# Optimization experiments

Measured on AMD Instinct MI355X. Metric: run time of the kernel, lower is better.

Reference implementation:

```python
import jax, jax.numpy as jnp
import numpy as np

# dims matching init_kwargs
L = 2          # lstm_depth
H = 512        # lstm_size
E = 512        # text_embedding_size
V = 32000      # vocab_size
FH = 512       # feature_embedding_hidden_size
FEAT = 2048    # feature_size
START_IDX = 3.0  # start_of_seq_token_idx (used as a fill value, per original code)


def _lstm_cell(x, h, c, Wih, Whh, b):
    # PyTorch gate order: i, f, g, o. Wih:[in,4H], Whh:[H,4H], b:[4H]
    gates = x @ Wih + h @ Whh + b  # [B,4H]
    i, f, g, o = jnp.split(gates, 4, axis=-1)
    c_new = jax.nn.sigmoid(f) * c + jax.nn.sigmoid(i) * jnp.tanh(g)
    h_new = jax.nn.sigmoid(o) * jnp.tanh(c_new)
    return h_new, c_new


def setup_inputs() -> dict:
    key = jax.random.key(0)
    ks = jax.random.split(key, 12)
    B, N, T = 64, 49, 40
    s = 0.02
    img_data = jax.random.normal(ks[0], (B, N, FEAT), jnp.float32)
    W_fh = jax.random.normal(ks[1], (FEAT, FH), jnp.float32) * s
    b_fh = jnp.zeros((FH,), jnp.float32)
    Wc = jax.random.normal(ks[2], (L, FH, H), jnp.float32) * s
    bc = jnp.zeros((L, H), jnp.float32)
    Wh = jax.random.normal(ks[3], (L, FH, H), jnp.float32) * s
    bh = jnp.zeros((L, H), jnp.float32)
    W_ih = jax.random.normal(ks[4], (L, E, 4 * H), jnp.float32) * 0.04
    W_hh = jax.random.normal(ks[5], (L, H, 4 * H), jnp.float32) * 0.04
    b_lstm = jnp.zeros((L, 4 * H), jnp.float32)
    emb = jax.random.normal(ks[6], (V, E), jnp.float32) * s
    u = jax.random.uniform(ks[7], (T, B, V), jnp.float32, minval=1e-6, maxval=1.0 - 1e-6)
    gumbel = -jnp.log(-jnp.log(u))  # Gumbel(0,1) noise: Gumbel-max == Categorical.sample
    return {
        "img_data": img_data, "W_fh": W_fh, "b_fh": b_fh,
        "Wc": Wc, "bc": bc, "Wh": Wh, "bh": bh,
        "W_ih": W_ih, "W_hh": W_hh, "b_lstm": b_lstm,
        "emb": emb, "gumbel": gumbel, "max_seq_len": 40,
    }


def reference(img_data, W_fh, b_fh, Wc, bc, Wh, bh, W_ih, W_hh, b_lstm, emb, gumbel, max_seq_len):
    B = img_data.shape[0]
    # f_embedding = tanh(Linear(img_data)) : [B,N,FH]
    f_emb = jnp.tanh(img_data @ W_fh + b_fh)
    # mean over regions commutes with the per-layer Linear: mean(f @ W + b) = mean(f) @ W + b
    f_mean = jnp.mean(f_emb, axis=1)  # [B,FH]
    c0 = jnp.einsum('bf,lfh->lbh', f_mean, Wc) + bc[:, None, :]  # [L,B,H]
    h0 = jnp.einsum('bf,lfh->lbh', f_mean, Wh) + bh[:, None, :]
    # initial "embedding" is zeros + start_of_seq_token_idx (a constant fill, per original)
    x0 = jnp.full((B, E), START_IDX, dtype=img_data.dtype)
    emb_T = emb.T  # [E,V]

    def step(carry, g_t):
        h, c, x = carry  # h,c:[L,B,H], x:[B,E]; g_t:[B,V]
        inp = x
        hs, cs = [], []
        for l in range(L):  # small static depth
            hn, cn = _lstm_cell(inp, h[l], c[l], W_ih[l], W_hh[l], b_lstm[l])
            hs.append(hn); cs.append(cn)
            inp = hn
        logits = inp @ emb_T                      # [B,V]
        logp = jax.nn.log_softmax(logits, axis=-1)
        tok = jnp.argmax(logp + g_t, axis=-1)     # Gumbel-max categorical sample
        lp = jnp.take_along_axis(logp, tok[:, None], axis=1)[:, 0]  # [B]
        x_next = emb[tok]                         # next-step embedding lookup
        return (jnp.stack(hs, 0), jnp.stack(cs, 0), x_next), (tok, lp)

    _, (tokens, log_probs) = jax.lax.scan(step, (h0, c0, x0), gumbel)
    return tokens.T, log_probs.T  # [B,T], [B,T]
```

## Files before the change

### kernel.cpp

```cpp
#include <hip/hip_runtime.h>
#include <cmath>

namespace {

constexpr int BATCH = 64;
constexpr int NREG  = 49;
constexpr int FEATN = 2048;
constexpr int FHN   = 512;
constexpr int HID   = 512;
constexpr int EMBN  = 512;
constexpr int VOC   = 32000;
constexpr int TSTEPS= 40;
constexpr int G4    = 2048;
constexpr int NVT   = VOC / 128;

typedef short bf16x8 __attribute__((ext_vector_type(8)));
typedef float f32x4  __attribute__((ext_vector_type(4)));

__device__ __forceinline__ float sigm(float x) { return 1.0f / (1.0f + expf(-x)); }

__device__ __forceinline__ unsigned short f2bf(float f) {
  unsigned u = __float_as_uint(f);
  unsigned r = (u + 0x7fffu + ((u >> 16) & 1u)) >> 16;
  return (unsigned short)r;
}

__device__ __forceinline__ bool better(float a, int ia, float b, int ib) {
  return a > b || (a == b && ia < ib);
}
__device__ __forceinline__ void top2_merge(float& v1, int& i1, float& v2, int& i2,
                                           float u1, int j1, float u2, int j2) {
  if (better(u1, j1, v1, i1)) {
    float t = v1; int ti = i1;
    v1 = u1; i1 = j1;
    if (better(u2, j2, t, ti)) { v2 = u2; i2 = j2; } else { v2 = t; i2 = ti; }
  } else {
    if (better(u1, j1, v2, i2)) { v2 = u1; i2 = j1; }
  }
}
__device__ __forceinline__ void lse_merge(float& m, float& s, float om, float os) {
  float nm = fmaxf(m, om);
  float ns = 0.f;
  if (m  > -INFINITY) ns += s  * expf(m  - nm);
  if (om > -INFINITY) ns += os * expf(om - nm);
  m = nm; s = ns;
}

__global__ __launch_bounds__(256) void k_feat(const float* __restrict__ img, const float* __restrict__ W,
                                              const float* __restrict__ bias, float* __restrict__ femb) {
  const int m0 = blockIdx.x * 64, n0 = blockIdx.y * 64;
  __shared__ float As[16][68];
  __shared__ float Bs[16][68];
  const int tid = threadIdx.x, tx = tid & 15, ty = tid >> 4;
  float acc[4][4] = {};
  for (int k0 = 0; k0 < FEATN; k0 += 16) {
#pragma unroll
    for (int e = 0; e < 4; ++e) {
      int idx = tid + e * 256, m = idx >> 4, k = idx & 15;
      As[k][m] = img[(size_t)(m0 + m) * FEATN + k0 + k];
    }
#pragma unroll
    for (int e = 0; e < 4; ++e) {
      int idx = tid + e * 256, k = idx >> 6, n = idx & 63;
      Bs[k][n] = W[(size_t)(k0 + k) * FHN + n0 + n];
    }
    __syncthreads();
#pragma unroll
    for (int k = 0; k < 16; ++k) {
      float4 av = *(const float4*)&As[k][ty * 4];
      float4 bv = *(const float4*)&Bs[k][tx * 4];
      float a[4] = {av.x, av.y, av.z, av.w}, b[4] = {bv.x, bv.y, bv.z, bv.w};
#pragma unroll
      for (int i = 0; i < 4; ++i)
#pragma unroll
        for (int j = 0; j < 4; ++j) acc[i][j] = fmaf(a[i], b[j], acc[i][j]);
    }
    __syncthreads();
  }
#pragma unroll
  for (int i = 0; i < 4; ++i) {
    int m = m0 + ty * 4 + i, n = n0 + tx * 4;
    float4 o;
    o.x = tanhf(acc[i][0] + bias[n + 0]);
    o.y = tanhf(acc[i][1] + bias[n + 1]);
    o.z = tanhf(acc[i][2] + bias[n + 2]);
    o.w = tanhf(acc[i][3] + bias[n + 3]);
    *(float4*)&femb[(size_t)m * FHN + n] = o;
  }
}

__global__ void k_mean(const float* __restrict__ femb, float* __restrict__ fmean) {
  const int gid = blockIdx.x * 256 + threadIdx.x;
  const int b = gid >> 9, f = gid & 511;
  float s = 0.f;
  for (int n = 0; n < NREG; ++n) s += femb[(size_t)(b * NREG + n) * FHN + f];
  fmean[gid] = s * (1.0f / NREG);
}

__global__ __launch_bounds__(256) void k_h0c0(const float* __restrict__ fmean,
    const float* __restrict__ Wc, const float* __restrict__ bc,
    const float* __restrict__ Wh, const float* __restrict__ bh,
    float* __restrict__ hbuf, float* __restrict__ cbuf) {
  const int n0 = blockIdx.x * 64, l = blockIdx.y, isH = blockIdx.z;
  const float* W   = (isH ? Wh : Wc) + (size_t)l * FHN * HID;
  const float* bias= (isH ? bh : bc) + l * HID;
  float* outp      = (isH ? hbuf : cbuf) + (size_t)l * BATCH * HID;
  __shared__ float As[16][68], Bs[16][68];
  const int tid = threadIdx.x, tx = tid & 15, ty = tid >> 4;
  float acc[4][4] = {};
  for (int k0 = 0; k0 < FHN; k0 += 16) {
#pragma unroll
    for (int e = 0; e < 4; ++e) { int idx = tid + e * 256, m = idx >> 4, k = idx & 15; As[k][m] = fmean[m * FHN + k0 + k]; }
#pragma unroll
    for (int e = 0; e < 4; ++e) { int idx = tid + e * 256, k = idx >> 6, n = idx & 63; Bs[k][n] = W[(size_t)(k0 + k) * HID + n0 + n]; }
    __syncthreads();
#pragma unroll
    for (int k = 0; k < 16; ++k) {
      float4 av = *(const float4*)&As[k][ty * 4];
      float4 bv = *(const float4*)&Bs[k][tx * 4];
      float a[4] = {av.x, av.y, av.z, av.w}, b[4] = {bv.x, bv.y, bv.z, bv.w};
#pragma unroll
      for (int i = 0; i < 4; ++i)
#pragma unroll
        for (int j = 0; j < 4; ++j) acc[i][j] = fmaf(a[i], b[j], acc[i][j]);
    }
    __syncthreads();
  }
#pragma unroll
  for (int i = 0; i < 4; ++i) {
    int m = ty * 4 + i, n = n0 + tx * 4;
    float4 o = make_float4(acc[i][0] + bias[n], acc[i][1] + bias[n + 1],
                           acc[i][2] + bias[n + 2], acc[i][3] + bias[n + 3]);
    *(float4*)&outp[(size_t)m * HID + n] = o;
  }
}

__global__ void k_init(float* __restrict__ xbuf) {
  xbuf[blockIdx.x * 256 + threadIdx.x] = 3.0f;
}

__global__ void k_emb2bf(const float* __restrict__ emb, unsigned short* __restrict__ ebf) {
  const int i = blockIdx.x * 256 + threadIdx.x;
  const float4* p = reinterpret_cast<const float4*>(emb) + (size_t)i * 2;
  float4 a = p[0], b = p[1];
  uint4 o;
  o.x = (unsigned)f2bf(a.x) | ((unsigned)f2bf(a.y) << 16);
  o.y = (unsigned)f2bf(a.z) | ((unsigned)f2bf(a.w) << 16);
  o.z = (unsigned)f2bf(b.x) | ((unsigned)f2bf(b.y) << 16);
  o.w = (unsigned)f2bf(b.z) | ((unsigned)f2bf(b.w) << 16);
  reinterpret_cast<uint4*>(ebf)[i] = o;
}

__global__ __launch_bounds__(256) void k_gates(const float* __restrict__ X, const float* __restrict__ Hs,
    const float* __restrict__ Wih, const float* __restrict__ Whh, float* __restrict__ part) {
  const int n0 = blockIdx.x * 64;
  const int ks = blockIdx.y;
  const float* A; const float* Wm; int kbase;
  if (ks < 4) { A = X;  Wm = Wih; kbase = ks * 128; }
  else        { A = Hs; Wm = Whh; kbase = (ks - 4) * 128; }
  __shared__ float As[16][68], Bs[16][68];
  const int tid = threadIdx.x, tx = tid & 15, ty = tid >> 4;
  float acc[4][4] = {};
  for (int kk = 0; kk < 128; kk += 16) {
    const int k0 = kbase + kk;
#pragma unroll
    for (int e = 0; e < 4; ++e) { int idx = tid + e * 256, m = idx >> 4, k = idx & 15; As[k][m] = A[m * EMBN + k0 + k]; }
#pragma unroll
    for (int e = 0; e < 4; ++e) { int idx = tid + e * 256, k = idx >> 6, n = idx & 63; Bs[k][n] = Wm[(size_t)(k0 + k) * G4 + n0 + n]; }
    __syncthreads();
#pragma unroll
    for (int k = 0; k < 16; ++k) {
      float4 av = *(const float4*)&As[k][ty * 4];
      float4 bvv = *(const float4*)&Bs[k][tx * 4];
      float a[4] = {av.x, av.y, av.z, av.w}, b[4] = {bvv.x, bvv.y, bvv.z, bvv.w};
#pragma unroll
      for (int i = 0; i < 4; ++i)
#pragma unroll
        for (int j = 0; j < 4; ++j) acc[i][j] = fmaf(a[i], b[j], acc[i][j]);
    }
    __syncthreads();
  }
  float* pp = part + (size_t)ks * BATCH * G4;
#pragma unroll
  for (int i = 0; i < 4; ++i) {
    int m = ty * 4 + i, n = n0 + tx * 4;
    *(float4*)&pp[(size_t)m * G4 + n] = make_float4(acc[i][0], acc[i][1], acc[i][2], acc[i][3]);
  }
}

__global__ void k_cell(const float* __restrict__ part, const float* __restrict__ bias,
                       float* __restrict__ h, float* __restrict__ c,
                       unsigned short* __restrict__ hbf) {
  const int gid = blockIdx.x * 256 + threadIdx.x;
  const int b = gid >> 9, j = gid & 511;
  float gi = bias[j], gf = bias[j + 512], gg = bias[j + 1024], go = bias[j + 1536];
#pragma unroll
  for (int ks = 0; ks < 8; ++ks) {
    const float* p = part + (size_t)ks * BATCH * G4 + (size_t)b * G4;
    gi += p[j]; gf += p[j + 512]; gg += p[j + 1024]; go += p[j + 1536];
  }
  float cn = sigm(gf) * c[gid] + sigm(gi) * tanhf(gg);
  float hn = sigm(go) * tanhf(cn);
  c[gid] = cn; h[gid] = hn;
  if (hbf) hbf[gid] = f2bf(hn);
}

__global__ __launch_bounds__(256) void k_logits_mfma(
    const unsigned short* __restrict__ embbf,
    const unsigned short* __restrict__ h1bf,
    const float* __restrict__ gum,
    float* __restrict__ red) {
  const int v0 = blockIdx.x * 128;
  const int tid = threadIdx.x;
  const int lane = tid & 63, w = tid >> 6;
  const int l15 = lane & 15, l4 = lane >> 4;

  __shared__ unsigned short hl[32768];
  __shared__ float rm_[256], rs_[256], rv1_[256], rv2_[256];
  __shared__ int   ri1_[256], ri2_[256];

#pragma unroll
  for (int i = 0; i < 16; ++i) {
    int c = tid + i * 256;
    int row = c >> 6;
    int inb = (c & 63) << 4;
    uint4 v = *reinterpret_cast<const uint4*>(h1bf + ((size_t)c << 3));
    int sw = inb ^ ((row & 7) << 4);
    *reinterpret_cast<uint4*>(reinterpret_cast<char*>(hl) + row * 1024 + sw) = v;
  }
  __syncthreads();

  f32x4 acc[2][4];
#pragma unroll
  for (int m = 0; m < 2; ++m)
#pragma unroll
    for (int n = 0; n < 4; ++n) acc[m][n] = (f32x4){0.f, 0.f, 0.f, 0.f};

  const unsigned short* aptr = embbf + (size_t)(v0 + w * 32 + l15) * 512 + l4 * 8;
#pragma unroll
  for (int ks = 0; ks < 16; ++ks) {
    bf16x8 a0 = *reinterpret_cast<const bf16x8*>(aptr + ks * 32);
    bf16x8 a1 = *reinterpret_cast<const bf16x8*>(aptr + 16 * 512 + ks * 32);
    bf16x8 bb[4];
#pragma unroll
    for (int n = 0; n < 4; ++n) {
      int row = n * 16 + l15;
      int inb = ks * 64 + l4 * 16;
      int sw = inb ^ ((row & 7) << 4);
      bb[n] = *reinterpret_cast<const bf16x8*>(reinterpret_cast<const char*>(hl) + row * 1024 + sw);
    }
#pragma unroll
    for (int n = 0; n < 4; ++n) {
      acc[0][n] = __builtin_amdgcn_mfma_f32_16x16x32_bf16(a0, bb[n], acc[0][n], 0, 0, 0);
      acc[1][n] = __builtin_amdgcn_mfma_f32_16x16x32_bf16(a1, bb[n], acc[1][n], 0, 0, 0);
    }
  }

  const int vb = v0 + w * 32 + l4 * 4;
#pragma unroll
  for (int n = 0; n < 4; ++n) {
    const int b = n * 16 + l15;
    const float* gb = gum + (size_t)b * VOC + vb;
    float4 g0 = *reinterpret_cast<const float4*>(gb);
    float4 g1 = *reinterpret_cast<const float4*>(gb + 16);
    float lg[8] = {acc[0][n][0], acc[0][n][1], acc[0][n][2], acc[0][n][3],
                   acc[1][n][0], acc[1][n][1], acc[1][n][2], acc[1][n][3]};
    float gv[8] = {g0.x, g0.y, g0.z, g0.w, g1.x, g1.y, g1.z, g1.w};
    float mx = lg[0];
#pragma unroll
    for (int i = 1; i < 8; ++i) mx = fmaxf(mx, lg[i]);
    float ss = 0.f;
    float v1 = -INFINITY, v2 = -INFINITY; int i1 = 0x7fffffff, i2 = 0x7fffffff;
#pragma unroll
    for (int i = 0; i < 8; ++i) {
      ss += expf(lg[i] - mx);
      float val = lg[i] + gv[i];
      int idx = vb + (i & 3) + ((i >> 2) << 4);
      if (better(val, idx, v1, i1)) { v2 = v1; i2 = i1; v1 = val; i1 = idx; }
      else if (better(val, idx, v2, i2)) { v2 = val; i2 = idx; }
    }
#pragma unroll
    for (int mask = 16; mask <= 32; mask <<= 1) {
      float om = __shfl_xor(mx, mask);
      float os = __shfl_xor(ss, mask);
      float u1 = __shfl_xor(v1, mask); int j1 = __shfl_xor(i1, mask);
      float u2 = __shfl_xor(v2, mask); int j2 = __shfl_xor(i2, mask);
      lse_merge(mx, ss, om, os);
      top2_merge(v1, i1, v2, i2, u1, j1, u2, j2);
    }
    if (lane < 16) {
      int slot = (w * 4 + n) * 16 + l15;
      rm_[slot] = mx; rs_[slot] = ss;
      rv1_[slot] = v1; ri1_[slot] = i1; rv2_[slot] = v2; ri2_[slot] = i2;
    }
  }
  __syncthreads();
  if (tid < 64) {
    const int n = tid >> 4, c = tid & 15;
    int s0 = n * 16 + c;
    float M = rm_[s0], S = rs_[s0], V1 = rv1_[s0], V2 = rv2_[s0];
    int I1 = ri1_[s0], I2 = ri2_[s0];
#pragma unroll
    for (int ww = 1; ww < 4; ++ww) {
      int sl = (ww * 4 + n) * 16 + c;
      lse_merge(M, S, rm_[sl], rs_[sl]);
      top2_merge(V1, I1, V2, I2, rv1_[sl], ri1_[sl], rv2_[sl], ri2_[sl]);
    }
    float* rp = red + ((size_t)blockIdx.x * 64 + tid) * 8;
    rp[0] = M; rp[1] = S;
    rp[2] = V1; rp[3] = __int_as_float(I1);
    rp[4] = V2; rp[5] = __int_as_float(I2);
  }
}

__global__ __launch_bounds__(256) void k_sample(const float* __restrict__ red,
    const float* __restrict__ emb, const float* __restrict__ h1f, const float* __restrict__ gum,
    float* __restrict__ xnext, float* __restrict__ out, int t) {
  const int b = blockIdx.x, tid = threadIdx.x;
  __shared__ float rm[256], rs[256], rv1[256], rv2[256];
  __shared__ int   ri1[256], ri2[256];
  float m = -INFINITY, s = 0.f, v1 = -INFINITY, v2 = -INFINITY;
  int i1 = 0x7fffffff, i2 = 0x7fffffff;
  if (tid < NVT) {
    const float* rp = red + ((size_t)tid * 64 + b) * 8;
    m = rp[0]; s = rp[1];
    v1 = rp[2]; i1 = __float_as_int(rp[3]);
    v2 = rp[4]; i2 = __float_as_int(rp[5]);
  }
  rm[tid] = m; rs[tid] = s; rv1[tid] = v1; ri1[tid] = i1; rv2[tid] = v2; ri2[tid] = i2;
  __syncthreads();
  for (int off = 128; off > 0; off >>= 1) {
    if (tid < off) {
      float M = rm[tid], S = rs[tid];
      lse_merge(M, S, rm[tid + off], rs[tid + off]);
      rm[tid] = M; rs[tid] = S;
      float a1 = rv1[tid], a2 = rv2[tid]; int c1 = ri1[tid], c2 = ri2[tid];
      top2_merge(a1, c1, a2, c2, rv1[tid + off], ri1[tid + off], rv2[tid + off], ri2[tid + off]);
      rv1[tid] = a1; ri1[tid] = c1; rv2[tid] = a2; ri2[tid] = c2;
    }
    __syncthreads();
  }
  const int I1 = ri1[0], I2 = ri2[0];
  const float lse = rm[0] + logf(rs[0]);
  __shared__ float s1[256], s2[256];
  const float* e1 = emb + (size_t)I1 * EMBN;
  const float* e2 = emb + (size_t)I2 * EMBN;
  const float* hb = h1f + b * EMBN;
  float d1 = 0.f, d2 = 0.f;
  for (int k = tid; k < EMBN; k += 256) {
    float hv = hb[k];
    d1 = fmaf(e1[k], hv, d1);
    d2 = fmaf(e2[k], hv, d2);
  }
  s1[tid] = d1; s2[tid] = d2;
  __syncthreads();
  for (int off = 128; off > 0; off >>= 1) {
    if (tid < off) { s1[tid] += s1[tid + off]; s2[tid] += s2[tid + off]; }
    __syncthreads();
  }
  const float x1 = s1[0] + gum[(size_t)b * VOC + I1];
  const float x2 = s2[0] + gum[(size_t)b * VOC + I2];
  int tok; float dsel;
  if (x2 > x1 || (x2 == x1 && I2 < I1)) { tok = I2; dsel = s2[0]; }
  else                                  { tok = I1; dsel = s1[0]; }
  const float* et = emb + (size_t)tok * EMBN;
  for (int k = tid; k < EMBN; k += 256) xnext[b * EMBN + k] = et[k];
  if (tid == 0) {
    out[b * TSTEPS + t] = (float)tok;
    out[BATCH * TSTEPS + b * TSTEPS + t] = dsel - lse;
  }
}

}

extern "C" void kernel_launch(void* const* d_in, const int* in_sizes, int n_in,
                              void* d_out, int out_size, void* d_ws, size_t ws_size,
                              hipStream_t stream) {
  const float* img  = (const float*)d_in[0];
  const float* W_fh = (const float*)d_in[1];
  const float* b_fh = (const float*)d_in[2];
  const float* Wc   = (const float*)d_in[3];
  const float* bc   = (const float*)d_in[4];
  const float* Wh   = (const float*)d_in[5];
  const float* bh   = (const float*)d_in[6];
  const float* W_ih = (const float*)d_in[7];
  const float* W_hh = (const float*)d_in[8];
  const float* b_l  = (const float*)d_in[9];
  const float* emb  = (const float*)d_in[10];
  const float* gum  = (const float*)d_in[11];
  float* out = (float*)d_out;

  float* w     = (float*)d_ws;
  float* femb  = w;
  float* fmean = femb + (size_t)3136 * 512;
  float* hbuf  = fmean + 64 * 512;
  float* cbuf  = hbuf + 2 * 64 * 512;
  float* xbuf  = cbuf + 2 * 64 * 512;
  float* part  = xbuf + 64 * 512;
  float* red   = part + (size_t)8 * 64 * 2048;
  unsigned short* embbf = (unsigned short*)(red + 250 * 64 * 8);
  unsigned short* h1bf  = embbf + (size_t)VOC * EMBN;

  k_feat<<<dim3(49, 8), 256, 0, stream>>>(img, W_fh, b_fh, femb);
  k_mean<<<128, 256, 0, stream>>>(femb, fmean);
  k_h0c0<<<dim3(8, 2, 2), 256, 0, stream>>>(fmean, Wc, bc, Wh, bh, hbuf, cbuf);
  k_init<<<128, 256, 0, stream>>>(xbuf);
  k_emb2bf<<<8000, 256, 0, stream>>>(emb, embbf);

  for (int t = 0; t < TSTEPS; ++t) {
    const float* gum_t = gum + (size_t)t * BATCH * VOC;
    k_gates<<<dim3(32, 8), 256, 0, stream>>>(xbuf, hbuf, W_ih, W_hh, part);
    k_cell<<<128, 256, 0, stream>>>(part, b_l, hbuf, cbuf, (unsigned short*)nullptr);
    k_gates<<<dim3(32, 8), 256, 0, stream>>>(hbuf, hbuf + 64 * 512,
                                             W_ih + (size_t)512 * 2048, W_hh + (size_t)512 * 2048, part);
    k_cell<<<128, 256, 0, stream>>>(part, b_l + 2048, hbuf + 64 * 512, cbuf + 64 * 512, h1bf);
    k_logits_mfma<<<NVT, 256, 0, stream>>>(embbf, h1bf, gum_t, red);
    k_sample<<<64, 256, 0, stream>>>(red, emb, hbuf + 64 * 512, gum_t, xbuf, out, t);
  }
}
```

Measured before the change: 2.216 ms.

## Use split-bf16 MFMA for feature and LSTM gate GEMMs

Replaces the fp32 FMA tiled GEMMs for the image-feature projection and the per-step LSTM gate matmuls with bf16 MFMA kernels. Precision is kept by splitting each operand into hi+lo bf16 parts and summing three products. Weights are pre-transposed and split once per call, and activations (x, h) are written as hi/lo bf16 by the producing kernels. This adds preprocessing passes over the image tensor and weights, plus extra workspace and memory traffic, in exchange for matrix-core throughput.

```diff
diff --git a/kernel.cpp b/kernel.cpp
--- a/kernel.cpp
+++ b/kernel.cpp
@@ -24,6 +24,9 @@
   unsigned r = (u + 0x7fffu + ((u >> 16) & 1u)) >> 16;
   return (unsigned short)r;
 }
+__device__ __forceinline__ float bf2f(unsigned short h) {
+  return __uint_as_float(((unsigned)h) << 16);
+}
 
 __device__ __forceinline__ bool better(float a, int ia, float b, int ib) {
   return a > b || (a == b && ia < ib);
@@ -46,47 +49,89 @@
   m = nm; s = ns;
 }
 
-__global__ __launch_bounds__(256) void k_feat(const float* __restrict__ img, const float* __restrict__ W,
-                                              const float* __restrict__ bias, float* __restrict__ femb) {
+__global__ __launch_bounds__(256) void k_trans(const float* __restrict__ src,
+    unsigned short* __restrict__ dhi, unsigned short* __restrict__ dlo, int K, int N) {
+  __shared__ float tile[32][33];
+  const int k0 = blockIdx.x * 32, n0 = blockIdx.y * 32;
+  const int tx = threadIdx.x & 31, ty = threadIdx.x >> 5;
+#pragma unroll
+  for (int r = ty; r < 32; r += 8) tile[r][tx] = src[(size_t)(k0 + r) * N + n0 + tx];
+  __syncthreads();
+#pragma unroll
+  for (int r = ty; r < 32; r += 8) {
+    float v = tile[tx][r];
+    unsigned short hv = f2bf(v);
+    size_t o = (size_t)(n0 + r) * K + k0 + tx;
+    dhi[o] = hv;
+    dlo[o] = f2bf(v - bf2f(hv));
+  }
+}
+
+__global__ void k_split(const float* __restrict__ src, unsigned short* __restrict__ dhi,
+                        unsigned short* __restrict__ dlo) {
+  const size_t i = (size_t)blockIdx.x * 256 + threadIdx.x;
+  const float4* p = reinterpret_cast<const float4*>(src) + i * 2;
+  float4 a = p[0], b = p[1];
+  float v[8] = {a.x, a.y, a.z, a.w, b.x, b.y, b.z, b.w};
+  unsigned short hi[8], lo[8];
+#pragma unroll
+  for (int j = 0; j < 8; ++j) {
+    hi[j] = f2bf(v[j]);
+    lo[j] = f2bf(v[j] - bf2f(hi[j]));
+  }
+  uint4 oh, ol;
+  oh.x = hi[0] | (hi[1] << 16); oh.y = hi[2] | (hi[3] << 16);
+  oh.z = hi[4] | (hi[5] << 16); oh.w = hi[6] | (hi[7] << 16);
+  ol.x = lo[0] | (lo[1] << 16); ol.y = lo[2] | (lo[3] << 16);
+  ol.z = lo[4] | (lo[5] << 16); ol.w = lo[6] | (lo[7] << 16);
+  reinterpret_cast<uint4*>(dhi)[i] = oh;
+  reinterpret_cast<uint4*>(dlo)[i] = ol;
+}
+
+__global__ void k_emb2bf(const float* __restrict__ emb, unsigned short* __restrict__ ebf) {
+  const size_t i = (size_t)blockIdx.x * 256 + threadIdx.x;
+  const float4* p = reinterpret_cast<const float4*>(emb) + i * 2;
+  float4 a = p[0], b = p[1];
+  uint4 o;
+  o.x = (unsigned)f2bf(a.x) | ((unsigned)f2bf(a.y) << 16);
+  o.y = (unsigned)f2bf(a.z) | ((unsigned)f2bf(a.w) << 16);
+  o.z = (unsigned)f2bf(b.x) | ((unsigned)f2bf(b.y) << 16);
+  o.w = (unsigned)f2bf(b.z) | ((unsigned)f2bf(b.w) << 16);
+  reinterpret_cast<uint4*>(ebf)[i] = o;
+}
+
+__global__ __launch_bounds__(256) void k_feat_mfma(
+    const unsigned short* __restrict__ Ahi, const unsigned short* __restrict__ Alo,
+    const unsigned short* __restrict__ Bhi, const unsigned short* __restrict__ Blo,
+    const float* __restrict__ bias, float* __restrict__ femb) {
   const int m0 = blockIdx.x * 64, n0 = blockIdx.y * 64;
-  __shared__ float As[16][68];
-  __shared__ float Bs[16][68];
-  const int tid = threadIdx.x, tx = tid & 15, ty = tid >> 4;
-  float acc[4][4] = {};
-  for (int k0 = 0; k0 < FEATN; k0 += 16) {
-#pragma unroll
-    for (int e = 0; e < 4; ++e) {
-      int idx = tid + e * 256, m = idx >> 4, k = idx & 15;
-      As[k][m] = img[(size_t)(m0 + m) * FEATN + k0 + k];
-    }
-#pragma unroll
-    for (int e = 0; e < 4; ++e) {
-      int idx = tid + e * 256, k = idx >> 6, n = idx & 63;
-      Bs[k][n] = W[(size_t)(k0 + k) * FHN + n0 + n];
-    }
-    __syncthreads();
-#pragma unroll
-    for (int k = 0; k < 16; ++k) {
-      float4 av = *(const float4*)&As[k][ty * 4];
-      float4 bv = *(const float4*)&Bs[k][tx * 4];
-      float a[4] = {av.x, av.y, av.z, av.w}, b[4] = {bv.x, bv.y, bv.z, bv.w};
-#pragma unroll
-      for (int i = 0; i < 4; ++i)
-#pragma unroll
-        for (int j = 0; j < 4; ++j) acc[i][j] = fmaf(a[i], b[j], acc[i][j]);
-    }
-    __syncthreads();
-  }
-#pragma unroll
-  for (int i = 0; i < 4; ++i) {
-    int m = m0 + ty * 4 + i, n = n0 + tx * 4;
-    float4 o;
-    o.x = tanhf(acc[i][0] + bias[n + 0]);
-    o.y = tanhf(acc[i][1] + bias[n + 1]);
-    o.z = tanhf(acc[i][2] + bias[n + 2]);
-    o.w = tanhf(acc[i][3] + bias[n + 3]);
-    *(float4*)&femb[(size_t)m * FHN + n] = o;
-  }
+  const int tid = threadIdx.x, lane = tid & 63, w = tid >> 6;
+  const int l15 = lane & 15, l4 = lane >> 4;
+  f32x4 acc[4];
+#pragma unroll
+  for (int nt = 0; nt < 4; ++nt) acc[nt] = (f32x4){0.f, 0.f, 0.f, 0.f};
+  const size_t arow = (size_t)(m0 + w * 16 + l15) * FEATN;
+  for (int kk = 0; kk < FEATN / 32; ++kk) {
+    const int k = kk * 32 + l4 * 8;
+    bf16x8 a1 = *reinterpret_cast<const bf16x8*>(Ahi + arow + k);
+    bf16x8 a2 = *reinterpret_cast<const bf16x8*>(Alo + arow + k);
+#pragma unroll
+    for (int nt = 0; nt < 4; ++nt) {
+      const size_t brow = (size_t)(n0 + nt * 16 + l15) * FEATN + k;
+      bf16x8 b1 = *reinterpret_cast<const bf16x8*>(Bhi + brow);
+      bf16x8 b2 = *reinterpret_cast<const bf16x8*>(Blo + brow);
+      acc[nt] = __builtin_amdgcn_mfma_f32_16x16x32_bf16(a1, b1, acc[nt], 0, 0, 0);
+      acc[nt] = __builtin_amdgcn_mfma_f32_16x16x32_bf16(a1, b2, acc[nt], 0, 0, 0);
+      acc[nt] = __builtin_amdgcn_mfma_f32_16x16x32_bf16(a2, b1, acc[nt], 0, 0, 0);
+    }
+  }
+#pragma unroll
+  for (int nt = 0; nt < 4; ++nt)
+#pragma unroll
+    for (int i = 0; i < 4; ++i) {
+      int m = m0 + w * 16 + l4 * 4 + i, n = n0 + nt * 16 + l15;
+      femb[(size_t)m * FHN + n] = tanhf(acc[nt][i] + bias[n]);
+    }
 }
 
 __global__ void k_mean(const float* __restrict__ femb, float* __restrict__ fmean) {
@@ -100,7 +145,8 @@
 __global__ __launch_bounds__(256) void k_h0c0(const float* __restrict__ fmean,
     const float* __restrict__ Wc, const float* __restrict__ bc,
     const float* __restrict__ Wh, const float* __restrict__ bh,
-    float* __restrict__ hbuf, float* __restrict__ cbuf) {
+    float* __restrict__ hbuf, float* __restrict__ cbuf,
+    unsigned short* __restrict__ hshi, unsigned short* __restrict__ hslo) {
   const int n0 = blockIdx.x * 64, l = blockIdx.y, isH = blockIdx.z;
   const float* W   = (isH ? Wh : Wc) + (size_t)l * FHN * HID;
   const float* bias= (isH ? bh : bc) + l * HID;
@@ -129,68 +175,73 @@
 #pragma unroll
   for (int i = 0; i < 4; ++i) {
     int m = ty * 4 + i, n = n0 + tx * 4;
-    float4 o = make_float4(acc[i][0] + bias[n], acc[i][1] + bias[n + 1],
-                           acc[i][2] + bias[n + 2], acc[i][3] + bias[n + 3]);
-    *(float4*)&outp[(size_t)m * HID + n] = o;
-  }
-}
-
-__global__ void k_init(float* __restrict__ xbuf) {
-  xbuf[blockIdx.x * 256 + threadIdx.x] = 3.0f;
-}
-
-__global__ void k_emb2bf(const float* __restrict__ emb, unsigned short* __restrict__ ebf) {
+    float vals[4];
+#pragma unroll
+    for (int j = 0; j < 4; ++j) vals[j] = acc[i][j] + bias[n + j];
+    *(float4*)&outp[(size_t)m * HID + n] = make_float4(vals[0], vals[1], vals[2], vals[3]);
+    if (isH) {
+#pragma unroll
+      for (int j = 0; j < 4; ++j) {
+        unsigned short hv = f2bf(vals[j]);
+        size_t o = (size_t)l * BATCH * HID + (size_t)m * HID + n + j;
+        hshi[o] = hv;
+        hslo[o] = f2bf(vals[j] - bf2f(hv));
+      }
+    }
+  }
+}
+
+__global__ void k_initx(unsigned short* __restrict__ xhi, unsigned short* __restrict__ xlo) {
   const int i = blockIdx.x * 256 + threadIdx.x;
-  const float4* p = reinterpret_cast<const float4*>(emb) + (size_t)i * 2;
-  float4 a = p[0], b = p[1];
-  uint4 o;
-  o.x = (unsigned)f2bf(a.x) | ((unsigned)f2bf(a.y) << 16);
-  o.y = (unsigned)f2bf(a.z) | ((unsigned)f2bf(a.w) << 16);
-  o.z = (unsigned)f2bf(b.x) | ((unsigned)f2bf(b.y) << 16);
-  o.w = (unsigned)f2bf(b.z) | ((unsigned)f2bf(b.w) << 16);
-  reinterpret_cast<uint4*>(ebf)[i] = o;
-}
-
-__global__ __launch_bounds__(256) void k_gates(const float* __restrict__ X, const float* __restrict__ Hs,
-    const float* __restrict__ Wih, const float* __restrict__ Whh, float* __restrict__ part) {
+  xhi[i] = 0x4040; xlo[i] = 0;
+}
+
+__global__ __launch_bounds__(256) void k_gates_mfma(
+    const unsigned short* __restrict__ xhi, const unsigned short* __restrict__ xlo,
+    const unsigned short* __restrict__ hhi, const unsigned short* __restrict__ hlo,
+    const unsigned short* __restrict__ wih_hi, const unsigned short* __restrict__ wih_lo,
+    const unsigned short* __restrict__ whh_hi, const unsigned short* __restrict__ whh_lo,
+    float* __restrict__ part) {
   const int n0 = blockIdx.x * 64;
   const int ks = blockIdx.y;
-  const float* A; const float* Wm; int kbase;
-  if (ks < 4) { A = X;  Wm = Wih; kbase = ks * 128; }
-  else        { A = Hs; Wm = Whh; kbase = (ks - 4) * 128; }
-  __shared__ float As[16][68], Bs[16][68];
-  const int tid = threadIdx.x, tx = tid & 15, ty = tid >> 4;
-  float acc[4][4] = {};
-  for (int kk = 0; kk < 128; kk += 16) {
-    const int k0 = kbase + kk;
-#pragma unroll
-    for (int e = 0; e < 4; ++e) { int idx = tid + e * 256, m = idx >> 4, k = idx & 15; As[k][m] = A[m * EMBN + k0 + k]; }
-#pragma unroll
-    for (int e = 0; e < 4; ++e) { int idx = tid + e * 256, k = idx >> 6, n = idx & 63; Bs[k][n] = Wm[(size_t)(k0 + k) * G4 + n0 + n]; }
-    __syncthreads();
-#pragma unroll
-    for (int k = 0; k < 16; ++k) {
-      float4 av = *(const float4*)&As[k][ty * 4];
-      float4 bvv = *(const float4*)&Bs[k][tx * 4];
-      float a[4] = {av.x, av.y, av.z, av.w}, b[4] = {bvv.x, bvv.y, bvv.z, bvv.w};
-#pragma unroll
-      for (int i = 0; i < 4; ++i)
-#pragma unroll
-        for (int j = 0; j < 4; ++j) acc[i][j] = fmaf(a[i], b[j], acc[i][j]);
-    }
-    __syncthreads();
+  const unsigned short *Ah, *Al, *Wh_, *Wl;
+  int kbase;
+  if (ks < 4) { Ah = xhi; Al = xlo; Wh_ = wih_hi; Wl = wih_lo; kbase = ks * 128; }
+  else        { Ah = hhi; Al = hlo; Wh_ = whh_hi; Wl = whh_lo; kbase = (ks - 4) * 128; }
+  const int tid = threadIdx.x, lane = tid & 63, w = tid >> 6;
+  const int l15 = lane & 15, l4 = lane >> 4;
+  f32x4 acc[4];
+#pragma unroll
+  for (int nt = 0; nt < 4; ++nt) acc[nt] = (f32x4){0.f, 0.f, 0.f, 0.f};
+  const size_t arow = (size_t)(w * 16 + l15) * EMBN;
+#pragma unroll
+  for (int kk = 0; kk < 4; ++kk) {
+    const int k = kbase + kk * 32 + l4 * 8;
+    bf16x8 a1 = *reinterpret_cast<const bf16x8*>(Ah + arow + k);
+    bf16x8 a2 = *reinterpret_cast<const bf16x8*>(Al + arow + k);
+#pragma unroll
+    for (int nt = 0; nt < 4; ++nt) {
+      const size_t brow = (size_t)(n0 + nt * 16 + l15) * EMBN + k;
+      bf16x8 b1 = *reinterpret_cast<const bf16x8*>(Wh_ + brow);
+      bf16x8 b2 = *reinterpret_cast<const bf16x8*>(Wl + brow);
+      acc[nt] = __builtin_amdgcn_mfma_f32_16x16x32_bf16(a1, b1, acc[nt], 0, 0, 0);
+      acc[nt] = __builtin_amdgcn_mfma_f32_16x16x32_bf16(a1, b2, acc[nt], 0, 0, 0);
+      acc[nt] = __builtin_amdgcn_mfma_f32_16x16x32_bf16(a2, b1, acc[nt], 0, 0, 0);
+    }
   }
   float* pp = part + (size_t)ks * BATCH * G4;
 #pragma unroll
-  for (int i = 0; i < 4; ++i) {
-    int m = ty * 4 + i, n = n0 + tx * 4;
-    *(float4*)&pp[(size_t)m * G4 + n] = make_float4(acc[i][0], acc[i][1], acc[i][2], acc[i][3]);
-  }
+  for (int nt = 0; nt < 4; ++nt)
+#pragma unroll
+    for (int i = 0; i < 4; ++i) {
+      int b = w * 16 + l4 * 4 + i, n = n0 + nt * 16 + l15;
+      pp[(size_t)b * G4 + n] = acc[nt][i];
+    }
 }
 
 __global__ void k_cell(const float* __restrict__ part, const float* __restrict__ bias,
                        float* __restrict__ h, float* __restrict__ c,
-                       unsigned short* __restrict__ hbf) {
+                       unsigned short* __restrict__ hhi, unsigned short* __restrict__ hlo) {
   const int gid = blockIdx.x * 256 + threadIdx.x;
   const int b = gid >> 9, j = gid & 511;
   float gi = bias[j], gf = bias[j + 512], gg = bias[j + 1024], go = bias[j + 1536];
@@ -202,7 +253,9 @@
   float cn = sigm(gf) * c[gid] + sigm(gi) * tanhf(gg);
   float hn = sigm(go) * tanhf(cn);
   c[gid] = cn; h[gid] = hn;
-  if (hbf) hbf[gid] = f2bf(hn);
+  unsigned short hv = f2bf(hn);
+  hhi[gid] = hv;
+  hlo[gid] = f2bf(hn - bf2f(hv));
 }
 
 __global__ __launch_bounds__(256) void k_logits_mfma(
@@ -315,7 +368,8 @@
 
 __global__ __launch_bounds__(256) void k_sample(const float* __restrict__ red,
     const float* __restrict__ emb, const float* __restrict__ h1f, const float* __restrict__ gum,
-    float* __restrict__ xnext, float* __restrict__ out, int t) {
+    unsigned short* __restrict__ xhi, unsigned short* __restrict__ xlo,
+    float* __restrict__ out, int t) {
   const int b = blockIdx.x, tid = threadIdx.x;
   __shared__ float rm[256], rs[256], rv1[256], rv2[256];
   __shared__ int   ri1[256], ri2[256];
@@ -364,7 +418,12 @@
   if (x2 > x1 || (x2 == x1 && I2 < I1)) { tok = I2; dsel = s2[0]; }
   else                                  { tok = I1; dsel = s1[0]; }
   const float* et = emb + (size_t)tok * EMBN;
-  for (int k = tid; k < EMBN; k += 256) xnext[b * EMBN + k] = et[k];
+  for (int k = tid; k < EMBN; k += 256) {
+    float ev = et[k];
+    unsigned short hv = f2bf(ev);
+    xhi[b * EMBN + k] = hv;
+    xlo[b * EMBN + k] = f2bf(ev - bf2f(hv));
+  }
   if (tid == 0) {
     out[b * TSTEPS + t] = (float)tok;
     out[BATCH * TSTEPS + b * TSTEPS + t] = dsel - lse;
@@ -395,26 +454,48 @@
   float* fmean = femb + (size_t)3136 * 512;
   float* hbuf  = fmean + 64 * 512;
   float* cbuf  = hbuf + 2 * 64 * 512;
-  float* xbuf  = cbuf + 2 * 64 * 512;
-  float* part  = xbuf + 64 * 512;
+  float* part  = cbuf + 2 * 64 * 512;
   float* red   = part + (size_t)8 * 64 * 2048;
-  unsigned short* embbf = (unsigned short*)(red + 250 * 64 * 8);
-  unsigned short* h1bf  = embbf + (size_t)VOC * EMBN;
-
-  k_feat<<<dim3(49, 8), 256, 0, stream>>>(img, W_fh, b_fh, femb);
+
+  unsigned short* us = (unsigned short*)(red + 250 * 64 * 8);
+  unsigned short* embbf  = us;
+  unsigned short* imghi  = embbf + (size_t)VOC * EMBN;
+  unsigned short* imglo  = imghi + (size_t)3136 * 2048;
+  unsigned short* wfh_hi = imglo + (size_t)3136 * 2048;
+  unsigned short* wfh_lo = wfh_hi + (size_t)512 * 2048;
+  unsigned short* wg     = wfh_lo + (size_t)512 * 2048;
+  const size_t WGM = (size_t)2048 * 512;
+  unsigned short* xhi    = wg + 8 * WGM;
+  unsigned short* xlo    = xhi + 64 * 512;
+  unsigned short* hshi   = xlo + 64 * 512;
+  unsigned short* hslo   = hshi + 2 * 64 * 512;
+
+  auto wgp = [&](int l, int mat, int part_) -> unsigned short* {
+    return wg + (((size_t)l * 2 + mat) * 2 + part_) * WGM;
+  };
+
+  k_emb2bf<<<8000, 256, 0, stream>>>(emb, embbf);
+  k_split<<<3136 * 2048 / 8 / 256, 256, 0, stream>>>(img, imghi, imglo);
+  k_trans<<<dim3(FEATN / 32, FHN / 32), 256, 0, stream>>>(W_fh, wfh_hi, wfh_lo, FEATN, FHN);
+  for (int l = 0; l < 2; ++l) {
+    k_trans<<<dim3(EMBN / 32, G4 / 32), 256, 0, stream>>>(W_ih + (size_t)l * EMBN * G4, wgp(l, 0, 0), wgp(l, 0, 1), EMBN, G4);
+    k_trans<<<dim3(HID / 32, G4 / 32), 256, 0, stream>>>(W_hh + (size_t)l * HID * G4, wgp(l, 1, 0), wgp(l, 1, 1), HID, G4);
+  }
+  k_feat_mfma<<<dim3(49, 8), 256, 0, stream>>>(imghi, imglo, wfh_hi, wfh_lo, b_fh, femb);
   k_mean<<<128, 256, 0, stream>>>(femb, fmean);
-  k_h0c0<<<dim3(8, 2, 2), 256, 0, stream>>>(fmean, Wc, bc, Wh, bh, hbuf, cbuf);
-  k_init<<<128, 256, 0, stream>>>(xbuf);
-  k_emb2bf<<<8000, 256, 0, stream>>>(emb, embbf);
+  k_h0c0<<<dim3(8, 2, 2), 256, 0, stream>>>(fmean, Wc, bc, Wh, bh, hbuf, cbuf, hshi, hslo);
+  k_initx<<<128, 256, 0, stream>>>(xhi, xlo);
 
   for (int t = 0; t < TSTEPS; ++t) {
     const float* gum_t = gum + (size_t)t * BATCH * VOC;
-    k_gates<<<dim3(32, 8), 256, 0, stream>>>(xbuf, hbuf, W_ih, W_hh, part);
-    k_cell<<<128, 256, 0, stream>>>(part, b_l, hbuf, cbuf, (unsigned short*)nullptr);
-    k_gates<<<dim3(32, 8), 256, 0, stream>>>(hbuf, hbuf + 64 * 512,
-                                             W_ih + (size_t)512 * 2048, W_hh + (size_t)512 * 2048, part);
-    k_cell<<<128, 256, 0, stream>>>(part, b_l + 2048, hbuf + 64 * 512, cbuf + 64 * 512, h1bf);
-    k_logits_mfma<<<NVT, 256, 0, stream>>>(embbf, h1bf, gum_t, red);
-    k_sample<<<64, 256, 0, stream>>>(red, emb, hbuf + 64 * 512, gum_t, xbuf, out, t);
-  }
-}
+    k_gates_mfma<<<dim3(32, 8), 256, 0, stream>>>(xhi, xlo, hshi, hslo,
+        wgp(0, 0, 0), wgp(0, 0, 1), wgp(0, 1, 0), wgp(0, 1, 1), part);
+    k_cell<<<128, 256, 0, stream>>>(part, b_l, hbuf, cbuf, hshi, hslo);
+    k_gates_mfma<<<dim3(32, 8), 256, 0, stream>>>(hshi, hslo, hshi + 64 * 512, hslo + 64 * 512,
+        wgp(1, 0, 0), wgp(1, 0, 1), wgp(1, 1, 0), wgp(1, 1, 1), part);
+    k_cell<<<128, 256, 0, stream>>>(part, b_l + 2048, hbuf + 64 * 512, cbuf + 64 * 512,
+                                    hshi + 64 * 512, hslo + 64 * 512);
+    k_logits_mfma<<<NVT, 256, 0, stream>>>(embbf, hshi + 64 * 512, gum_t, red);
+    k_sample<<<64, 256, 0, stream>>>(red, emb, hbuf + 64 * 512, gum_t, xhi, xlo, out, t);
+  }
+}
```

After: 2.040 ms. -7.9%, faster.
